# Kernel tuning notes

Measured on AMD Instinct MI355X. Metric: run time of the kernel, lower is better.

## Reference

```python
import jax, jax.numpy as jnp
import numpy as np

IN_FILTERS = 512
SIM_DIM = 128
LOOKUP = 101
OUT_DIM = 128


def setup_inputs() -> dict:
    key = jax.random.key(0)
    k1, k2, k3, k4 = jax.random.split(key, 4)
    x = jax.random.normal(k1, (4, IN_FILTERS, 1024, 8, 8), dtype=jnp.float32)
    # nn.Linear weights: [out, in]
    W_proj = jax.random.normal(k2, (SIM_DIM, IN_FILTERS), dtype=jnp.float32) * (1.0 / np.sqrt(IN_FILTERS))
    W_fc = jax.random.normal(k3, (OUT_DIM, LOOKUP), dtype=jnp.float32) * (1.0 / np.sqrt(LOOKUP))
    b_fc = jax.random.normal(k4, (OUT_DIM,), dtype=jnp.float32) * 0.01
    return {"x": x, "W_proj": W_proj, "W_fc": W_fc, "b_fc": b_fc}


def reference(x, W_proj, W_fc, b_fc):
    # x: [B, C, T, H, W]; inputs list has a single entry here, cat is identity
    feat = jnp.mean(x, axis=(3, 4))              # [B, C, T]
    feat = jnp.transpose(feat, (0, 2, 1))        # [B, T, C]
    p = jnp.einsum('btc,dc->btd', feat, W_proj)  # projection, no bias
    # F.normalize(p, p=2, dim=2) with eps=1e-12
    norm = jnp.linalg.norm(p, axis=2, keepdims=True)
    p = p / jnp.maximum(norm, 1e-12)
    B, T, _ = p.shape
    sim = jnp.einsum('btd,bsd->bts', p, p)       # full TxT similarity [B,T,T]
    half = (LOOKUP - 1) // 2
    sim_pad = jnp.pad(sim, ((0, 0), (0, 0), (half, half)))
    # band gather: row t takes padded cols [t, t+LOOKUP)
    cols = jnp.arange(T)[:, None] + jnp.arange(LOOKUP)[None, :]  # [T, L]
    band = sim_pad[:, jnp.arange(T)[:, None], cols]              # [B, T, L]
    out = jnp.einsum('btl,ol->bto', band, W_fc) + b_fc
    return jax.nn.relu(out)
```

## Files before the change

### kernel.cpp

```cpp
#include <hip/hip_runtime.h>
#include <cstdint>
#include <cstddef>

#define B_DIM 4
#define C_DIM 512
#define T_DIM 1024
#define D_DIM 128
#define L_DIM 101
#define O_DIM 128

__global__ __launch_bounds__(256) void pool_kernel(const float* __restrict__ x,
                                                   float* __restrict__ feat) {
    const int bt  = blockIdx.x;
    const int b   = bt >> 10;
    const int t   = bt & (T_DIM - 1);
    const int tid = threadIdx.x;
    const int sub = tid & 15;
    const int gi  = tid >> 4;
    __shared__ float feat_s[C_DIM];

    #pragma unroll 4
    for (int it = 0; it < C_DIM / 16; ++it) {
        const int c = it * 16 + gi;
        const size_t gidx = ((((size_t)b * C_DIM + c) * T_DIM + t) << 6) + (sub << 2);
        const float4 v = *(const float4*)(x + gidx);
        float s = v.x + v.y + v.z + v.w;
        s += __shfl_down(s, 8, 16);
        s += __shfl_down(s, 4, 16);
        s += __shfl_down(s, 2, 16);
        s += __shfl_down(s, 1, 16);
        if (sub == 0) feat_s[c] = s * (1.0f / 64.0f);
    }
    __syncthreads();
    if (tid < C_DIM / 4) {
        ((float4*)(feat + (size_t)bt * C_DIM))[tid] = ((const float4*)feat_s)[tid];
    }
}

#define K2_ROWS 16
#define K2_KT 64
#define BS_STRIDE 132

__global__ __launch_bounds__(256) void proj_norm_kernel(const float* __restrict__ feat,
                                                        const float* __restrict__ Wp,
                                                        float* __restrict__ p) {
    __shared__ float As[K2_ROWS * K2_KT];
    __shared__ float Bs[K2_KT * BS_STRIDE];
    const int tid  = threadIdx.x;
    const int row0 = blockIdx.x * K2_ROWS;
    const int tr   = tid >> 5;
    const int tc   = tid & 31;
    const int r0   = tr * 2;
    const int c0   = tc * 4;

    float acc0[4] = {0.f, 0.f, 0.f, 0.f};
    float acc1[4] = {0.f, 0.f, 0.f, 0.f};

    for (int kt = 0; kt < C_DIM / K2_KT; ++kt) {
        const int k0 = kt * K2_KT;
        {
            const int i  = tid >> 4;
            const int k4 = (tid & 15) << 2;
            *(float4*)(As + i * K2_KT + k4) =
                *(const float4*)(feat + (size_t)(row0 + i) * C_DIM + k0 + k4);
        }
        #pragma unroll
        for (int j = 0; j < 8; ++j) {
            const int idx = tid + (j << 8);
            const int d   = idx >> 4;
            const int kk  = (idx & 15) << 2;
            const float4 v = *(const float4*)(Wp + (size_t)d * C_DIM + k0 + kk);
            Bs[(kk + 0) * BS_STRIDE + d] = v.x;
            Bs[(kk + 1) * BS_STRIDE + d] = v.y;
            Bs[(kk + 2) * BS_STRIDE + d] = v.z;
            Bs[(kk + 3) * BS_STRIDE + d] = v.w;
        }
        __syncthreads();
        #pragma unroll 8
        for (int k = 0; k < K2_KT; ++k) {
            const float a0 = As[(r0 + 0) * K2_KT + k];
            const float a1 = As[(r0 + 1) * K2_KT + k];
            const float4 b4 = *(const float4*)(Bs + k * BS_STRIDE + c0);
            acc0[0] += a0 * b4.x; acc0[1] += a0 * b4.y;
            acc0[2] += a0 * b4.z; acc0[3] += a0 * b4.w;
            acc1[0] += a1 * b4.x; acc1[1] += a1 * b4.y;
            acc1[2] += a1 * b4.z; acc1[3] += a1 * b4.w;
        }
        __syncthreads();
    }

    float ss0 = acc0[0]*acc0[0] + acc0[1]*acc0[1] + acc0[2]*acc0[2] + acc0[3]*acc0[3];
    float ss1 = acc1[0]*acc1[0] + acc1[1]*acc1[1] + acc1[2]*acc1[2] + acc1[3]*acc1[3];
    #pragma unroll
    for (int off = 16; off >= 1; off >>= 1) {
        ss0 += __shfl_xor(ss0, off, 32);
        ss1 += __shfl_xor(ss1, off, 32);
    }
    const float inv0 = 1.0f / fmaxf(sqrtf(ss0), 1e-12f);
    const float inv1 = 1.0f / fmaxf(sqrtf(ss1), 1e-12f);
    const float4 o0 = make_float4(acc0[0]*inv0, acc0[1]*inv0, acc0[2]*inv0, acc0[3]*inv0);
    const float4 o1 = make_float4(acc1[0]*inv1, acc1[1]*inv1, acc1[2]*inv1, acc1[3]*inv1);
    *(float4*)(p + (size_t)(row0 + r0 + 0) * D_DIM + c0) = o0;
    *(float4*)(p + (size_t)(row0 + r0 + 1) * D_DIM + c0) = o1;
}

#define TT 16
#define P_STRIDE 129
#define NROWS (TT + 100)

__global__ __launch_bounds__(256) void band_kernel(const float* __restrict__ p,
                                                   float* __restrict__ band) {
    __shared__ float p_s[NROWS * P_STRIDE];
    const int tid = threadIdx.x;
    const int b   = blockIdx.x >> 6;
    const int t0  = (blockIdx.x & 63) * TT;

    for (int idx = tid; idx < NROWS * (D_DIM / 4); idx += 256) {
        const int i  = idx >> 5;
        const int k4 = (idx & 31) << 2;
        const int r  = t0 - 50 + i;
        float4 v = make_float4(0.f, 0.f, 0.f, 0.f);
        if (r >= 0 && r < T_DIM)
            v = *(const float4*)(p + (size_t)((b << 10) + r) * D_DIM + k4);
        float* dst = p_s + i * P_STRIDE + k4;
        dst[0] = v.x; dst[1] = v.y; dst[2] = v.z; dst[3] = v.w;
    }
    __syncthreads();

    const size_t base = (size_t)((b << 10) + t0) * L_DIM;
    for (int idx = tid; idx < TT * L_DIM; idx += 256) {
        const int t = idx / L_DIM;
        const int l = idx - t * L_DIM;
        const float* pa = p_s + (t + 50) * P_STRIDE;
        const float* pb = p_s + (t + l) * P_STRIDE;
        float s = 0.f;
        #pragma unroll 8
        for (int k = 0; k < D_DIM; ++k) s += pa[k] * pb[k];
        band[base + idx] = s;
    }
}

__global__ __launch_bounds__(256) void fc_kernel(const float* __restrict__ band,
                                                 const float* __restrict__ Wfc,
                                                 const float* __restrict__ bfc,
                                                 float* __restrict__ out) {
    __shared__ float wfc_s[O_DIM * L_DIM];
    __shared__ float band_s[TT * L_DIM];
    const int tid = threadIdx.x;
    const int b   = blockIdx.x >> 6;
    const int t0  = (blockIdx.x & 63) * TT;
    const size_t base = (size_t)((b << 10) + t0) * L_DIM;

    for (int idx = tid; idx < O_DIM * L_DIM; idx += 256) wfc_s[idx] = Wfc[idx];
    for (int idx = tid; idx < TT * L_DIM; idx += 256)    band_s[idx] = band[base + idx];
    __syncthreads();

    const int o  = tid & 127;
    const int th = tid >> 7;
    const float bias = bfc[o];
    const float* w = wfc_s + o * L_DIM;
    #pragma unroll
    for (int pass = 0; pass < TT / 2; ++pass) {
        const int t = pass * 2 + th;
        const float* bd = band_s + t * L_DIM;
        float acc = bias;
        for (int l = 0; l < L_DIM; ++l) acc += bd[l] * w[l];
        out[(size_t)((b << 10) + t0 + t) * O_DIM + o] = fmaxf(acc, 0.f);
    }
}

extern "C" void kernel_launch(void* const* d_in, const int* in_sizes, int n_in,
                              void* d_out, int out_size, void* d_ws, size_t ws_size,
                              hipStream_t stream) {
    const float* x   = (const float*)d_in[0];
    const float* Wp  = (const float*)d_in[1];
    const float* Wfc = (const float*)d_in[2];
    const float* bfc = (const float*)d_in[3];
    float* out = (float*)d_out;

    char* ws = (char*)d_ws;
    float* feat = (float*)(ws);
    float* p    = (float*)(ws + (size_t)8  * 1024 * 1024);
    float* band = (float*)(ws + (size_t)10 * 1024 * 1024);

    pool_kernel<<<B_DIM * T_DIM, 256, 0, stream>>>(x, feat);
    proj_norm_kernel<<<(B_DIM * T_DIM) / K2_ROWS, 256, 0, stream>>>(feat, Wp, p);
    band_kernel<<<B_DIM * (T_DIM / TT), 256, 0, stream>>>(p, band);
    fc_kernel<<<B_DIM * (T_DIM / TT), 256, 0, stream>>>(band, Wfc, bfc, out);
}
```

Measured before the change: 748.6 us.

## Fuse pooling with projection and band similarity with FC layer

Merges the pooling and projection+normalize kernels into one, computing 4 time rows per block and reading a pre-transposed projection weight from global memory, so the intermediate feature buffer is no longer written and re-read. Fuses the band-similarity and FC kernels, keeping band values in shared memory and reusing the same shared buffer for the FC weights, which removes the band round-trip through global memory. It also halves the band tile to 8 rows so there are more blocks, and computes two band columns per thread. The cost is more redundant reloading of the FC weights and neighbouring p rows per block, plus an extra small transpose kernel.

```diff
diff --git a/kernel.cpp b/kernel.cpp
--- a/kernel.cpp
+++ b/kernel.cpp
@@ -9,164 +9,189 @@
 #define L_DIM 101
 #define O_DIM 128
 
-__global__ __launch_bounds__(256) void pool_kernel(const float* __restrict__ x,
-                                                   float* __restrict__ feat) {
-    const int bt  = blockIdx.x;
-    const int b   = bt >> 10;
-    const int t   = bt & (T_DIM - 1);
+__global__ __launch_bounds__(256) void wpt_kernel(const float* __restrict__ Wp,
+                                                  float* __restrict__ WpT) {
+    const int idx = blockIdx.x * 256 + threadIdx.x;
+    const int c = idx >> 7;
+    const int d = idx & 127;
+    WpT[idx] = Wp[d * C_DIM + c];
+}
+
+#define ROWS 4
+__global__ __launch_bounds__(256) void pool_proj_kernel(const float* __restrict__ x,
+                                                        const float* __restrict__ WpT,
+                                                        float* __restrict__ p) {
+    __shared__ float feat_s[ROWS * C_DIM];
+    __shared__ float red_s[8 * ROWS * D_DIM];
+    __shared__ float nrm_s[ROWS * 2];
     const int tid = threadIdx.x;
-    const int sub = tid & 15;
-    const int gi  = tid >> 4;
-    __shared__ float feat_s[C_DIM];
-
-    #pragma unroll 4
-    for (int it = 0; it < C_DIM / 16; ++it) {
-        const int c = it * 16 + gi;
-        const size_t gidx = ((((size_t)b * C_DIM + c) * T_DIM + t) << 6) + (sub << 2);
-        const float4 v = *(const float4*)(x + gidx);
-        float s = v.x + v.y + v.z + v.w;
-        s += __shfl_down(s, 8, 16);
-        s += __shfl_down(s, 4, 16);
-        s += __shfl_down(s, 2, 16);
-        s += __shfl_down(s, 1, 16);
-        if (sub == 0) feat_s[c] = s * (1.0f / 64.0f);
-    }
-    __syncthreads();
-    if (tid < C_DIM / 4) {
-        ((float4*)(feat + (size_t)bt * C_DIM))[tid] = ((const float4*)feat_s)[tid];
-    }
-}
-
-#define K2_ROWS 16
-#define K2_KT 64
-#define BS_STRIDE 132
-
-__global__ __launch_bounds__(256) void proj_norm_kernel(const float* __restrict__ feat,
-                                                        const float* __restrict__ Wp,
-                                                        float* __restrict__ p) {
-    __shared__ float As[K2_ROWS * K2_KT];
-    __shared__ float Bs[K2_KT * BS_STRIDE];
-    const int tid  = threadIdx.x;
-    const int row0 = blockIdx.x * K2_ROWS;
-    const int tr   = tid >> 5;
-    const int tc   = tid & 31;
-    const int r0   = tr * 2;
-    const int c0   = tc * 4;
-
-    float acc0[4] = {0.f, 0.f, 0.f, 0.f};
-    float acc1[4] = {0.f, 0.f, 0.f, 0.f};
-
-    for (int kt = 0; kt < C_DIM / K2_KT; ++kt) {
-        const int k0 = kt * K2_KT;
-        {
-            const int i  = tid >> 4;
-            const int k4 = (tid & 15) << 2;
-            *(float4*)(As + i * K2_KT + k4) =
-                *(const float4*)(feat + (size_t)(row0 + i) * C_DIM + k0 + k4);
-        }
+    const int bt0 = blockIdx.x * ROWS;
+    const int b   = bt0 >> 10;
+    const int t0  = bt0 & (T_DIM - 1);
+
+    {
+        const int sub = tid & 15;
+        const int grp = tid >> 4;
+        #pragma unroll 4
+        for (int it = 0; it < (ROWS * C_DIM) / 16; ++it) {
+            const int idx = it * 16 + grp;
+            const int row = idx >> 9;
+            const int c   = idx & (C_DIM - 1);
+            const size_t gidx =
+                ((((size_t)b * C_DIM + c) * T_DIM + (t0 + row)) << 6) + (sub << 2);
+            const float4 v = *(const float4*)(x + gidx);
+            float s = v.x + v.y + v.z + v.w;
+            s += __shfl_down(s, 8, 16);
+            s += __shfl_down(s, 4, 16);
+            s += __shfl_down(s, 2, 16);
+            s += __shfl_down(s, 1, 16);
+            if (sub == 0) feat_s[idx] = s * (1.0f / 64.0f);
+        }
+    }
+    __syncthreads();
+
+    {
+        const int lane4 = (tid & 31) << 2;
+        const int strm  = tid >> 5;
+        float a0[4] = {0,0,0,0}, a1[4] = {0,0,0,0}, a2[4] = {0,0,0,0}, a3[4] = {0,0,0,0};
+        for (int ci = 0; ci < C_DIM / 8; ++ci) {
+            const int c = ci * 8 + strm;
+            const float4 w = *(const float4*)(WpT + (size_t)c * D_DIM + lane4);
+            const float f0 = feat_s[0 * C_DIM + c];
+            const float f1 = feat_s[1 * C_DIM + c];
+            const float f2 = feat_s[2 * C_DIM + c];
+            const float f3 = feat_s[3 * C_DIM + c];
+            a0[0] += f0 * w.x; a0[1] += f0 * w.y; a0[2] += f0 * w.z; a0[3] += f0 * w.w;
+            a1[0] += f1 * w.x; a1[1] += f1 * w.y; a1[2] += f1 * w.z; a1[3] += f1 * w.w;
+            a2[0] += f2 * w.x; a2[1] += f2 * w.y; a2[2] += f2 * w.z; a2[3] += f2 * w.w;
+            a3[0] += f3 * w.x; a3[1] += f3 * w.y; a3[2] += f3 * w.z; a3[3] += f3 * w.w;
+        }
+        float* rb = red_s + strm * (ROWS * D_DIM) + lane4;
+        *(float4*)(rb + 0 * D_DIM) = make_float4(a0[0], a0[1], a0[2], a0[3]);
+        *(float4*)(rb + 1 * D_DIM) = make_float4(a1[0], a1[1], a1[2], a1[3]);
+        *(float4*)(rb + 2 * D_DIM) = make_float4(a2[0], a2[1], a2[2], a2[3]);
+        *(float4*)(rb + 3 * D_DIM) = make_float4(a3[0], a3[1], a3[2], a3[3]);
+    }
+    __syncthreads();
+
+    float pv[2];
+    const int lane = tid & 63;
+    const int wv   = tid >> 6;
+    #pragma unroll
+    for (int j = 0; j < 2; ++j) {
+        const int idx = j * 256 + tid;
+        const int rd  = idx;
+        float v = 0.f;
         #pragma unroll
-        for (int j = 0; j < 8; ++j) {
-            const int idx = tid + (j << 8);
-            const int d   = idx >> 4;
-            const int kk  = (idx & 15) << 2;
-            const float4 v = *(const float4*)(Wp + (size_t)d * C_DIM + k0 + kk);
-            Bs[(kk + 0) * BS_STRIDE + d] = v.x;
-            Bs[(kk + 1) * BS_STRIDE + d] = v.y;
-            Bs[(kk + 2) * BS_STRIDE + d] = v.z;
-            Bs[(kk + 3) * BS_STRIDE + d] = v.w;
-        }
-        __syncthreads();
-        #pragma unroll 8
-        for (int k = 0; k < K2_KT; ++k) {
-            const float a0 = As[(r0 + 0) * K2_KT + k];
-            const float a1 = As[(r0 + 1) * K2_KT + k];
-            const float4 b4 = *(const float4*)(Bs + k * BS_STRIDE + c0);
-            acc0[0] += a0 * b4.x; acc0[1] += a0 * b4.y;
-            acc0[2] += a0 * b4.z; acc0[3] += a0 * b4.w;
-            acc1[0] += a1 * b4.x; acc1[1] += a1 * b4.y;
-            acc1[2] += a1 * b4.z; acc1[3] += a1 * b4.w;
-        }
-        __syncthreads();
-    }
-
-    float ss0 = acc0[0]*acc0[0] + acc0[1]*acc0[1] + acc0[2]*acc0[2] + acc0[3]*acc0[3];
-    float ss1 = acc1[0]*acc1[0] + acc1[1]*acc1[1] + acc1[2]*acc1[2] + acc1[3]*acc1[3];
-    #pragma unroll
-    for (int off = 16; off >= 1; off >>= 1) {
-        ss0 += __shfl_xor(ss0, off, 32);
-        ss1 += __shfl_xor(ss1, off, 32);
-    }
-    const float inv0 = 1.0f / fmaxf(sqrtf(ss0), 1e-12f);
-    const float inv1 = 1.0f / fmaxf(sqrtf(ss1), 1e-12f);
-    const float4 o0 = make_float4(acc0[0]*inv0, acc0[1]*inv0, acc0[2]*inv0, acc0[3]*inv0);
-    const float4 o1 = make_float4(acc1[0]*inv1, acc1[1]*inv1, acc1[2]*inv1, acc1[3]*inv1);
-    *(float4*)(p + (size_t)(row0 + r0 + 0) * D_DIM + c0) = o0;
-    *(float4*)(p + (size_t)(row0 + r0 + 1) * D_DIM + c0) = o1;
-}
-
-#define TT 16
-#define P_STRIDE 129
-#define NROWS (TT + 100)
-
-__global__ __launch_bounds__(256) void band_kernel(const float* __restrict__ p,
-                                                   float* __restrict__ band) {
-    __shared__ float p_s[NROWS * P_STRIDE];
+        for (int s = 0; s < 8; ++s) v += red_s[s * (ROWS * D_DIM) + rd];
+        pv[j] = v;
+        float ss = v * v;
+        ss += __shfl_xor(ss, 32, 64);
+        ss += __shfl_xor(ss, 16, 64);
+        ss += __shfl_xor(ss,  8, 64);
+        ss += __shfl_xor(ss,  4, 64);
+        ss += __shfl_xor(ss,  2, 64);
+        ss += __shfl_xor(ss,  1, 64);
+        if (lane == 0) {
+            const int row  = (j * 4 + wv) >> 1;
+            const int half = wv & 1;
+            nrm_s[row * 2 + half] = ss;
+        }
+    }
+    __syncthreads();
+    #pragma unroll
+    for (int j = 0; j < 2; ++j) {
+        const int idx = j * 256 + tid;
+        const int row = idx >> 7;
+        const int d   = idx & 127;
+        const float ss  = nrm_s[row * 2] + nrm_s[row * 2 + 1];
+        const float inv = 1.0f / fmaxf(sqrtf(ss), 1e-12f);
+        p[(size_t)(bt0 + row) * D_DIM + d] = pv[j] * inv;
+    }
+}
+
+#define TT 8
+#define PS 129
+#define NR 109
+#define SMEM_F (NR * PS)
+
+__global__ __launch_bounds__(256) void band_fc_kernel(const float* __restrict__ p,
+                                                      const float* __restrict__ Wfc,
+                                                      const float* __restrict__ bfc,
+                                                      float* __restrict__ out) {
+    __shared__ float smem[SMEM_F];
+    float* p_s = smem;
     const int tid = threadIdx.x;
-    const int b   = blockIdx.x >> 6;
-    const int t0  = (blockIdx.x & 63) * TT;
-
-    for (int idx = tid; idx < NROWS * (D_DIM / 4); idx += 256) {
+    const int b   = blockIdx.x >> 7;
+    const int t0  = (blockIdx.x & 127) * TT;
+
+    for (int idx = tid; idx < NR * (D_DIM / 4); idx += 256) {
         const int i  = idx >> 5;
         const int k4 = (idx & 31) << 2;
         const int r  = t0 - 50 + i;
         float4 v = make_float4(0.f, 0.f, 0.f, 0.f);
         if (r >= 0 && r < T_DIM)
             v = *(const float4*)(p + (size_t)((b << 10) + r) * D_DIM + k4);
-        float* dst = p_s + i * P_STRIDE + k4;
+        float* dst = p_s + i * PS + k4;
         dst[0] = v.x; dst[1] = v.y; dst[2] = v.z; dst[3] = v.w;
     }
     __syncthreads();
 
-    const size_t base = (size_t)((b << 10) + t0) * L_DIM;
-    for (int idx = tid; idx < TT * L_DIM; idx += 256) {
-        const int t = idx / L_DIM;
-        const int l = idx - t * L_DIM;
-        const float* pa = p_s + (t + 50) * P_STRIDE;
-        const float* pb = p_s + (t + l) * P_STRIDE;
-        float s = 0.f;
+    float s0[2], s1[2];
+    int ti[2], l0i[2];
+    #pragma unroll
+    for (int j = 0; j < 2; ++j) {
+        int idx = j * 256 + tid;
+        const bool valid = idx < TT * 51;
+        if (!valid) idx = 0;
+        const int t  = idx / 51;
+        const int lp = idx - t * 51;
+        ti[j]  = valid ? t : -1;
+        l0i[j] = lp * 2;
+        const float* pa  = p_s + (t + 50) * PS;
+        const float* pb0 = p_s + (t + lp * 2) * PS;
+        const float* pb1 = pb0 + PS;
+        float a0 = 0.f, a1 = 0.f;
         #pragma unroll 8
-        for (int k = 0; k < D_DIM; ++k) s += pa[k] * pb[k];
-        band[base + idx] = s;
-    }
-}
-
-__global__ __launch_bounds__(256) void fc_kernel(const float* __restrict__ band,
-                                                 const float* __restrict__ Wfc,
-                                                 const float* __restrict__ bfc,
-                                                 float* __restrict__ out) {
-    __shared__ float wfc_s[O_DIM * L_DIM];
-    __shared__ float band_s[TT * L_DIM];
-    const int tid = threadIdx.x;
-    const int b   = blockIdx.x >> 6;
-    const int t0  = (blockIdx.x & 63) * TT;
-    const size_t base = (size_t)((b << 10) + t0) * L_DIM;
-
-    for (int idx = tid; idx < O_DIM * L_DIM; idx += 256) wfc_s[idx] = Wfc[idx];
-    for (int idx = tid; idx < TT * L_DIM; idx += 256)    band_s[idx] = band[base + idx];
+        for (int k = 0; k < D_DIM; ++k) {
+            const float a = pa[k];
+            a0 += a * pb0[k];
+            a1 += a * pb1[k];
+        }
+        s0[j] = a0; s1[j] = a1;
+    }
+    __syncthreads();
+
+    float* band_s = smem;
+    float* wfc_s  = smem + TT * L_DIM;
+    #pragma unroll
+    for (int j = 0; j < 2; ++j) {
+        if (ti[j] >= 0) {
+            const int base = ti[j] * L_DIM + l0i[j];
+            band_s[base] = s0[j];
+            if (l0i[j] + 1 < L_DIM) band_s[base + 1] = s1[j];
+        }
+    }
+    for (int i = tid; i < O_DIM * L_DIM; i += 256) wfc_s[i] = Wfc[i];
     __syncthreads();
 
     const int o  = tid & 127;
     const int th = tid >> 7;
     const float bias = bfc[o];
-    const float* w = wfc_s + o * L_DIM;
-    #pragma unroll
-    for (int pass = 0; pass < TT / 2; ++pass) {
-        const int t = pass * 2 + th;
-        const float* bd = band_s + t * L_DIM;
-        float acc = bias;
-        for (int l = 0; l < L_DIM; ++l) acc += bd[l] * w[l];
-        out[(size_t)((b << 10) + t0 + t) * O_DIM + o] = fmaxf(acc, 0.f);
-    }
+    float acc[4] = {bias, bias, bias, bias};
+    const float* w  = wfc_s + o * L_DIM;
+    const float* bd = band_s + (th * 4) * L_DIM;
+    for (int l = 0; l < L_DIM; ++l) {
+        const float wv = w[l];
+        acc[0] += bd[0 * L_DIM + l] * wv;
+        acc[1] += bd[1 * L_DIM + l] * wv;
+        acc[2] += bd[2 * L_DIM + l] * wv;
+        acc[3] += bd[3 * L_DIM + l] * wv;
+    }
+    const size_t obase = (size_t)((b << 10) + t0 + th * 4) * O_DIM + o;
+    #pragma unroll
+    for (int r = 0; r < 4; ++r)
+        out[obase + (size_t)r * O_DIM] = fmaxf(acc[r], 0.f);
 }
 
 extern "C" void kernel_launch(void* const* d_in, const int* in_sizes, int n_in,
@@ -179,12 +204,10 @@
     float* out = (float*)d_out;
 
     char* ws = (char*)d_ws;
-    float* feat = (float*)(ws);
-    float* p    = (float*)(ws + (size_t)8  * 1024 * 1024);
-    float* band = (float*)(ws + (size_t)10 * 1024 * 1024);
-
-    pool_kernel<<<B_DIM * T_DIM, 256, 0, stream>>>(x, feat);
-    proj_norm_kernel<<<(B_DIM * T_DIM) / K2_ROWS, 256, 0, stream>>>(feat, Wp, p);
-    band_kernel<<<B_DIM * (T_DIM / TT), 256, 0, stream>>>(p, band);
-    fc_kernel<<<B_DIM * (T_DIM / TT), 256, 0, stream>>>(band, Wfc, bfc, out);
-}
+    float* WpT = (float*)(ws);
+    float* p   = (float*)(ws + (size_t)1024 * 1024);
+
+    wpt_kernel<<<(C_DIM * D_DIM) / 256, 256, 0, stream>>>(Wp, WpT);
+    pool_proj_kernel<<<(B_DIM * T_DIM) / ROWS, 256, 0, stream>>>(x, WpT, p);
+    band_fc_kernel<<<B_DIM * (T_DIM / TT), 256, 0, stream>>>(p, Wfc, bfc, out);
+}
```

Measured after the change: 715.9 us. 4.4% less time.
